# Optimization experiments

Measured on AMD Instinct MI355X. Metric: run time of the kernel, lower is better.

## Reference

```python
import jax, jax.numpy as jnp
import numpy as np

B, IN_DIM, UNITS = 16384, 3072, 3072  # batch, input_dim=3*unit1, units=3*unit2


def setup_inputs() -> dict:
    key = jax.random.key(0)
    k1, k2, k3 = jax.random.split(key, 3)
    inputs = jax.random.normal(k1, (B, IN_DIM), dtype=jnp.float32)
    # original init: uniform [0, 0.01) for w, zeros for b (gpe_bias = [0, 0])
    w = jax.random.uniform(k2, (IN_DIM, UNITS), dtype=jnp.float32, minval=0.0, maxval=0.01)
    b = jnp.zeros((UNITS,), dtype=jnp.float32)
    # per-unit binary diagonal mask, stored as [units, input_dim]
    mask = jax.random.randint(k3, (UNITS, IN_DIM), 0, 2, dtype=jnp.int32)
    return {"inputs": inputs, "w": w, "b": b, "mask": mask}


def reference(inputs, w, b, mask):
    # Original: p = transpose(s @ inputs^T, [2,0,1]) -> [batch, units, input_dim]
    #           f = diag_part(p @ w) + b            -> [batch, units]
    # Since s[u] = diag(mask[u]), this is exactly:
    #   f[b,u] = sum_i inputs[b,i] * mask[u,i] * w[i,u] + b[u]
    # i.e. a single masked GEMM with effective weight w * mask^T.
    w_eff = w * mask.T.astype(w.dtype)  # [input_dim, units]
    return inputs @ w_eff + b
```

## Files before the change

kernel.cpp:

```cpp
#include <hip/hip_runtime.h>

#define BATCH 16384
#define KDIM  3072
#define NDIM  3072

typedef __bf16 bf16;
typedef bf16  bf16x8 __attribute__((ext_vector_type(8)));
typedef float f32x4  __attribute__((ext_vector_type(4)));

__device__ __forceinline__ void g2l16(const bf16* g, bf16* l) {
    __builtin_amdgcn_global_load_lds(
        (__attribute__((address_space(1))) unsigned int*)g,
        (__attribute__((address_space(3))) unsigned int*)l,
        16, 0, 0);
}

__global__ __launch_bounds__(256) void cvt_a_kernel(const float* __restrict__ in,
                                                    bf16* __restrict__ out) {
    const long idx = (long)blockIdx.x * 256 + threadIdx.x;
    const float4* in4 = (const float4*)in;
    float4 a = in4[idx * 2];
    float4 b = in4[idx * 2 + 1];
    bf16x8 o;
    o[0] = (bf16)a.x; o[1] = (bf16)a.y; o[2] = (bf16)a.z; o[3] = (bf16)a.w;
    o[4] = (bf16)b.x; o[5] = (bf16)b.y; o[6] = (bf16)b.z; o[7] = (bf16)b.w;
    ((bf16x8*)out)[idx] = o;
}

__global__ __launch_bounds__(256) void weff_kernel(const float* __restrict__ w,
                                                   const int* __restrict__ mask,
                                                   bf16* __restrict__ wt) {
    __shared__ float tile[32][33];
    const int i0 = blockIdx.x * 32;
    const int u0 = blockIdx.y * 32;
    const int tx = threadIdx.x, ty = threadIdx.y;
#pragma unroll
    for (int r = 0; r < 4; r++)
        tile[ty + 8 * r][tx] = w[(long)(i0 + ty + 8 * r) * NDIM + u0 + tx];
    __syncthreads();
#pragma unroll
    for (int r = 0; r < 4; r++) {
        int u = u0 + ty + 8 * r;
        int i = i0 + tx;
        float v = tile[tx][ty + 8 * r] * (float)mask[(long)u * KDIM + i];
        wt[(long)u * KDIM + i] = (bf16)v;
    }
}

__global__ __launch_bounds__(256) void gemm_kernel(const bf16* __restrict__ A,
                                                   const bf16* __restrict__ Bt,
                                                   const float* __restrict__ bias,
                                                   float* __restrict__ C) {
    __shared__ __align__(16) bf16 lds[8192];

    const int tid  = threadIdx.x;
    const int lane = tid & 63;
    const int wv   = tid >> 6;
    const long m0 = (long)blockIdx.y * 128;
    const long n0 = (long)blockIdx.x * 128;
    const int waveM = (wv >> 1) * 64;
    const int waveN = (wv & 1) * 64;

    const bf16* gA = A + (m0 + (tid >> 2)) * KDIM + (tid & 3) * 8;
    const bf16* gB = Bt + (n0 + (tid >> 2)) * KDIM + (tid & 3) * 8;
    bf16* lA = &lds[tid * 8];
    bf16* lB = &lds[4096 + tid * 8];

    const int kq = (lane >> 4) * 8;
    const bf16* fA = &lds[(waveM + (lane & 15)) * 32 + kq];
    const bf16* fB = &lds[4096 + (waveN + (lane & 15)) * 32 + kq];

    f32x4 acc[4][4] = {};

    for (int k0 = 0; k0 < KDIM; k0 += 32) {
        __syncthreads();
        g2l16(gA, lA);
        g2l16(gA + 64 * KDIM, lA + 2048);
        g2l16(gB, lB);
        g2l16(gB + 64 * KDIM, lB + 2048);
        gA += 32;
        gB += 32;
        __syncthreads();

        bf16x8 af[4], bfr[4];
#pragma unroll
        for (int i = 0; i < 4; i++) af[i] = *(const bf16x8*)(fA + i * 512);
#pragma unroll
        for (int i = 0; i < 4; i++) bfr[i] = *(const bf16x8*)(fB + i * 512);
#pragma unroll
        for (int mi = 0; mi < 4; mi++)
#pragma unroll
            for (int ni = 0; ni < 4; ni++)
                acc[mi][ni] = __builtin_amdgcn_mfma_f32_16x16x32_bf16(
                    af[mi], bfr[ni], acc[mi][ni], 0, 0, 0);
    }

#pragma unroll
    for (int mi = 0; mi < 4; mi++) {
#pragma unroll
        for (int ni = 0; ni < 4; ni++) {
            const long r = m0 + waveM + mi * 16 + (lane >> 4) * 4;
            const long c = n0 + waveN + ni * 16 + (lane & 15);
            const float bv = bias[c];
#pragma unroll
            for (int reg = 0; reg < 4; reg++)
                C[(r + reg) * NDIM + c] = acc[mi][ni][reg] + bv;
        }
    }
}

__global__ __launch_bounds__(256) void naive_kernel(const float* __restrict__ x,
                                                    const float* __restrict__ w,
                                                    const float* __restrict__ bias,
                                                    const int* __restrict__ mask,
                                                    float* __restrict__ out) {
    const long idx = (long)blockIdx.x * 256 + threadIdx.x;
    const long bi = idx / NDIM;
    const int u = (int)(idx % NDIM);
    float s = 0.f;
    for (int k = 0; k < KDIM; k++)
        s += x[bi * KDIM + k] * w[(long)k * NDIM + u] * (float)mask[(long)u * KDIM + k];
    out[idx] = s + bias[u];
}

extern "C" void kernel_launch(void* const* d_in, const int* in_sizes, int n_in,
                              void* d_out, int out_size, void* d_ws, size_t ws_size,
                              hipStream_t stream) {
    const float* x    = (const float*)d_in[0];
    const float* w    = (const float*)d_in[1];
    const float* bias = (const float*)d_in[2];
    const int*   mask = (const int*)d_in[3];
    float* out = (float*)d_out;

    const size_t needA = (size_t)BATCH * KDIM * sizeof(bf16);
    const size_t needW = (size_t)NDIM * KDIM * sizeof(bf16);

    if (ws_size < needA + needW) {
        const long total = (long)BATCH * NDIM;
        naive_kernel<<<(int)(total / 256), 256, 0, stream>>>(x, w, bias, mask, out);
        return;
    }

    bf16* Abf = (bf16*)d_ws;
    bf16* Wt  = (bf16*)((char*)d_ws + needA);

    cvt_a_kernel<<<(BATCH * (KDIM / 8)) / 256, 256, 0, stream>>>(x, Abf);
    weff_kernel<<<dim3(KDIM / 32, NDIM / 32), dim3(32, 8), 0, stream>>>(w, mask, Wt);
    gemm_kernel<<<dim3(NDIM / 128, BATCH / 128), 256, 0, stream>>>(Abf, Wt, bias, out);
}
```

Measured before the change: 727.5 us.

## Switch GEMM to 32x32x16 MFMA with XOR-swizzled LDS layout

Replaces the 16x16x32 bf16 MFMA tiling (4x4 per wave) with 32x32x16 MFMA (2x2 per wave, two k-steps each), which reduces LDS fragment loads per MFMA and uses the larger matrix instruction. It also XOR-swizzles the 16-byte chunk placement in LDS on both the global-to-LDS copy and the fragment reads, to avoid bank conflicts from the new 32-row access pattern. The epilogue is rewritten for the 32x32 accumulator layout. The single-buffered, two-barrier K loop is unchanged, so latency hiding stays limited.

```diff
diff --git a/kernel.cpp b/kernel.cpp
--- a/kernel.cpp
+++ b/kernel.cpp
@@ -5,8 +5,8 @@
 #define NDIM  3072
 
 typedef __bf16 bf16;
-typedef bf16  bf16x8 __attribute__((ext_vector_type(8)));
-typedef float f32x4  __attribute__((ext_vector_type(4)));
+typedef bf16  bf16x8  __attribute__((ext_vector_type(8)));
+typedef float f32x16  __attribute__((ext_vector_type(16)));
 
 __device__ __forceinline__ void g2l16(const bf16* g, bf16* l) {
     __builtin_amdgcn_global_load_lds(
@@ -61,16 +61,22 @@
     const int waveM = (wv >> 1) * 64;
     const int waveN = (wv & 1) * 64;
 
-    const bf16* gA = A + (m0 + (tid >> 2)) * KDIM + (tid & 3) * 8;
-    const bf16* gB = Bt + (n0 + (tid >> 2)) * KDIM + (tid & 3) * 8;
+    const int srow   = tid >> 2;
+    const int schunk = (tid & 3) ^ ((tid >> 3) & 3);
+    const bf16* gA = A + (m0 + srow) * KDIM + schunk * 8;
+    const bf16* gB = Bt + (n0 + srow) * KDIM + schunk * 8;
     bf16* lA = &lds[tid * 8];
     bf16* lB = &lds[4096 + tid * 8];
 
-    const int kq = (lane >> 4) * 8;
-    const bf16* fA = &lds[(waveM + (lane & 15)) * 32 + kq];
-    const bf16* fB = &lds[4096 + (waveN + (lane & 15)) * 32 + kq];
+    const int rl  = lane & 31;
+    const int kb  = lane >> 5;
+    const int rsw = (rl >> 1) & 3;
+    const bf16* fA0 = &lds[(waveM + rl) * 32];
+    const bf16* fB0 = &lds[4096 + (waveN + rl) * 32];
+    const int c0 = ((0 + kb) ^ rsw) * 8;
+    const int c1 = ((2 + kb) ^ rsw) * 8;
 
-    f32x4 acc[4][4] = {};
+    f32x16 acc[2][2] = {};
 
     for (int k0 = 0; k0 < KDIM; k0 += 32) {
         __syncthreads();
@@ -82,29 +88,40 @@
         gB += 32;
         __syncthreads();
 
-        bf16x8 af[4], bfr[4];
+        bf16x8 a0[2], a1[2], b0[2], b1[2];
 #pragma unroll
-        for (int i = 0; i < 4; i++) af[i] = *(const bf16x8*)(fA + i * 512);
+        for (int mi = 0; mi < 2; mi++) {
+            a0[mi] = *(const bf16x8*)(fA0 + mi * 1024 + c0);
+            a1[mi] = *(const bf16x8*)(fA0 + mi * 1024 + c1);
+        }
 #pragma unroll
-        for (int i = 0; i < 4; i++) bfr[i] = *(const bf16x8*)(fB + i * 512);
+        for (int ni = 0; ni < 2; ni++) {
+            b0[ni] = *(const bf16x8*)(fB0 + ni * 1024 + c0);
+            b1[ni] = *(const bf16x8*)(fB0 + ni * 1024 + c1);
+        }
 #pragma unroll
-        for (int mi = 0; mi < 4; mi++)
+        for (int mi = 0; mi < 2; mi++)
 #pragma unroll
-            for (int ni = 0; ni < 4; ni++)
-                acc[mi][ni] = __builtin_amdgcn_mfma_f32_16x16x32_bf16(
-                    af[mi], bfr[ni], acc[mi][ni], 0, 0, 0);
+            for (int ni = 0; ni < 2; ni++) {
+                acc[mi][ni] = __builtin_amdgcn_mfma_f32_32x32x16_bf16(
+                    a0[mi], b0[ni], acc[mi][ni], 0, 0, 0);
+                acc[mi][ni] = __builtin_amdgcn_mfma_f32_32x32x16_bf16(
+                    a1[mi], b1[ni], acc[mi][ni], 0, 0, 0);
+            }
     }
 
 #pragma unroll
-    for (int mi = 0; mi < 4; mi++) {
+    for (int mi = 0; mi < 2; mi++) {
 #pragma unroll
-        for (int ni = 0; ni < 4; ni++) {
-            const long r = m0 + waveM + mi * 16 + (lane >> 4) * 4;
-            const long c = n0 + waveN + ni * 16 + (lane & 15);
-            const float bv = bias[c];
+        for (int ni = 0; ni < 2; ni++) {
+            const long col  = n0 + waveN + ni * 32 + rl;
+            const long rbase = m0 + waveM + mi * 32 + 4 * kb;
+            const float bv = bias[col];
 #pragma unroll
-            for (int reg = 0; reg < 4; reg++)
-                C[(r + reg) * NDIM + c] = acc[mi][ni][reg] + bv;
+            for (int g = 0; g < 4; g++)
+#pragma unroll
+                for (int t = 0; t < 4; t++)
+                    C[(rbase + 8 * g + t) * NDIM + col] = acc[mi][ni][4 * g + t] + bv;
         }
     }
 }
```

Result: no change. 733.8 us (+0.9%).
